# Kernel tuning notes

Measured on AMD Instinct MI355X. Metric: run time of the kernel, lower is better.

Reference implementation:

```python
import jax, jax.numpy as jnp
import numpy as np

NUM_EMBEDDINGS = 1024
EMBEDDING_DIM = 128
COMMITMENT_COEF = 0.25
DECAY = 0.99
EPS = 1e-5


def setup_inputs() -> dict:
    key = jax.random.key(0)
    k1, k2 = jax.random.split(key)
    z_e = jax.random.normal(k1, (64, EMBEDDING_DIM, 32, 32), dtype=jnp.float32)
    lim = 1.0 / NUM_EMBEDDINGS
    embed = jax.random.uniform(k2, (NUM_EMBEDDINGS, EMBEDDING_DIM), dtype=jnp.float32,
                               minval=-lim, maxval=lim)
    ema_cluster_size = jnp.zeros((NUM_EMBEDDINGS,), dtype=jnp.float32)
    ema_w = embed.copy()  # buffer initialized as clone of embed weights
    return {"z_e": z_e, "embed": embed,
            "ema_cluster_size": ema_cluster_size, "ema_w": ema_w}


def reference(z_e, embed, ema_cluster_size, ema_w):
    B, D, H, W = z_e.shape
    K = embed.shape[0]
    # [B,D,H,W] -> [N,D]
    flat = jnp.transpose(z_e, (0, 2, 3, 1)).reshape(-1, D)
    distances = (jnp.sum(flat ** 2, axis=1, keepdims=True)
                 + jnp.sum(embed ** 2, axis=1)
                 - 2.0 * jnp.matmul(flat, embed.T))
    encoding_indices = jnp.argmin(distances, axis=1)  # [N]

    quantized = embed[encoding_indices].reshape(B, H, W, D)
    quantized = jnp.transpose(quantized, (0, 3, 1, 2))  # [B,D,H,W]

    # ---- EMA codebook update (training path) ----
    N = flat.shape[0]
    cluster_size = jax.ops.segment_sum(jnp.ones((N,), flat.dtype),
                                       encoding_indices, num_segments=K)
    new_ema_cluster_size = DECAY * ema_cluster_size + (1.0 - DECAY) * cluster_size
    dw = jax.ops.segment_sum(flat, encoding_indices, num_segments=K)  # encodings^T @ flat
    new_ema_w = DECAY * ema_w + (1.0 - DECAY) * dw
    n = jnp.sum(new_ema_cluster_size)
    cs = (new_ema_cluster_size + EPS) / (n + K * EPS) * n
    new_embed = new_ema_w / cs[:, None]

    commitment_loss = jnp.mean((jax.lax.stop_gradient(quantized) - z_e) ** 2)
    loss = commitment_loss * COMMITMENT_COEF
    # straight-through estimator
    quantized_st = z_e + jax.lax.stop_gradient(quantized - z_e)
    indices = encoding_indices.reshape(B, H * W)
    return (quantized_st, indices, loss, new_embed, new_ema_cluster_size, new_ema_w)
```

## Files before the change

### kernel.cpp

```cpp
#include <hip/hip_runtime.h>

#define K_CODES 1024
#define DIM 128
#define HW 1024
#define NTOT 65536
#define DECAY 0.99f
#define OMD 0.01f
#define EPS 1e-5f
#define CCOEF 0.25f
#define MARGIN 1e-4f
#define FLCAP 24576

#define OFF_Q    0
#define OFF_IDX  8388608
#define OFF_LOSS (8388608 + 65536)
#define OFF_EMB  (OFF_LOSS + 1)
#define OFF_ECS  (OFF_EMB + 131072)
#define OFF_EMAW (OFF_ECS + 1024)

#define W_NORM2 0
#define W_RCP   1024
#define W_HIST  2048
#define W_LOSS  3072
#define W_FLCNT 3073
#define W_CNT2  3076
#define W_FL    (3076 + 24576)
#define W_M1F   (27652 + 24576)
#define W_CAND  (52228 + 24576)
#define W_EH    (76804 + 196608)
#define W_EL    (273412 + 65536)
#define W_NXIDX (338948 + 65536)
#define W_FLAT  (404484 + 65536)
#define W_NEED  (470020 + 8388608)

typedef __attribute__((ext_vector_type(8))) short short8v;
typedef __attribute__((ext_vector_type(4))) float f32x4;

__device__ __forceinline__ unsigned short f2bf(float f) {
    unsigned u = __float_as_uint(f);
    u += 0x7fffu + ((u >> 16) & 1u);
    return (unsigned short)(u >> 16);
}
__device__ __forceinline__ float bf2f(unsigned short h) {
    return __uint_as_float(((unsigned)h) << 16);
}

__global__ __launch_bounds__(256) void kzero(float* __restrict__ p, int n) {
    int i = blockIdx.x * 256 + threadIdx.x;
    if (i < n) p[i] = 0.f;
}

__device__ __forceinline__ float np_pairwise_sumsq_128(const float* p, size_t stride) {
    float r[8][4];
    #pragma unroll
    for (int j = 0; j < 8; ++j)
        #pragma unroll
        for (int L = 0; L < 4; ++L) {
            float x = p[(size_t)(j * 4 + L) * stride];
            r[j][L] = __fmul_rn(x, x);
        }
    #pragma unroll
    for (int c = 1; c < 4; ++c)
        #pragma unroll
        for (int j = 0; j < 8; ++j)
            #pragma unroll
            for (int L = 0; L < 4; ++L) {
                float x = p[(size_t)(c * 32 + j * 4 + L) * stride];
                r[j][L] = __fadd_rn(r[j][L], __fmul_rn(x, x));
            }
    float V[4];
    #pragma unroll
    for (int L = 0; L < 4; ++L) {
        float a = __fadd_rn(r[0][L], r[1][L]);
        float b = __fadd_rn(r[2][L], r[3][L]);
        float c2 = __fadd_rn(r[4][L], r[5][L]);
        float d2 = __fadd_rn(r[6][L], r[7][L]);
        V[L] = __fadd_rn(__fadd_rn(a, b), __fadd_rn(c2, d2));
    }
    return __fadd_rn(__fadd_rn(V[0], V[1]), __fadd_rn(V[2], V[3]));
}

__global__ __launch_bounds__(256) void kprep(
    const float* __restrict__ embed, float* __restrict__ norm2,
    unsigned short* __restrict__ ehs_g, unsigned short* __restrict__ els_g,
    float* __restrict__ zero_p, int zero_n)
{
    const int tid = threadIdx.x;
    const int bid = blockIdx.x;
    int zi = bid * 256 + tid;
    if (zi < zero_n) zero_p[zi] = 0.f;
    {
        const int g32 = tid >> 5, l32 = tid & 31;
        const int k = bid * 8 + g32;
        const float* row = embed + (size_t)k * DIM;
        float x = row[l32];
        float r = __fmul_rn(x, x);
        #pragma unroll
        for (int c = 1; c < 4; ++c) {
            float y = row[c * 32 + l32];
            r = __fadd_rn(r, __fmul_rn(y, y));
        }
        float s1 = __fadd_rn(r, __shfl_xor(r, 4, 64));
        float s2 = __fadd_rn(s1, __shfl_xor(s1, 8, 64));
        float s3 = __fadd_rn(s2, __shfl_xor(s2, 16, 64));
        float h1 = __fadd_rn(s3, __shfl_xor(s3, 1, 64));
        float h2 = __fadd_rn(h1, __shfl_xor(h1, 2, 64));
        if (l32 == 0) norm2[k] = h2;
    }
    if (ehs_g) {
        int hu = bid * 256 + tid;
        int U = hu >> 1, half = hu & 1;
        int code = U >> 4;
        int g = (U & 15) ^ (code & 15);
        const float* src = embed + (size_t)code * DIM + g * 8 + half * 4;
        float4 f = *(const float4*)src;
        unsigned short a = f2bf(f.x), b = f2bf(f.y), c = f2bf(f.z), d = f2bf(f.w);
        ushort4 hi; hi.x = a; hi.y = b; hi.z = c; hi.w = d;
        ushort4 lo;
        lo.x = f2bf(f.x - bf2f(a)); lo.y = f2bf(f.y - bf2f(b));
        lo.z = f2bf(f.z - bf2f(c)); lo.w = f2bf(f.w - bf2f(d));
        *(ushort4*)(ehs_g + (size_t)U * 8 + half * 4) = hi;
        *(ushort4*)(els_g + (size_t)U * 8 + half * 4) = lo;
    }
}

__global__ __launch_bounds__(256) void knx(const float* __restrict__ ze,
                                           float* __restrict__ nx,
                                           float* __restrict__ flat_c) {
    __shared__ float t[128][133];
    const int tid = threadIdx.x;
    const int n0 = blockIdx.x * 128;
    const int b = n0 >> 10, hw0 = n0 & (HW - 1);
    const float* zb = ze + (size_t)b * (DIM * HW) + hw0;
    #pragma unroll
    for (int i = 0; i < 64; ++i) {
        int d = i * 2 + (tid >> 7);
        int hw = tid & 127;
        t[hw][d] = zb[(size_t)d * HW + hw];
    }
    __syncthreads();
    if (tid < 128) nx[n0 + tid] = np_pairwise_sumsq_128(&t[tid][0], 1);
    if (flat_c) {
        #pragma unroll
        for (int i = 0; i < 16; ++i) {
            int lin = i * 256 + tid;
            int r  = lin >> 5;
            int c4 = lin & 31;
            float4 v = *(const float4*)&t[r][c4 * 4];
            *(float4*)&flat_c[(size_t)(n0 + r) * DIM + c4 * 4] = v;
        }
    }
}

__global__ __launch_bounds__(256, 4) void kapprox(
    const float* __restrict__ flat_c, const unsigned short* __restrict__ eh_g,
    const unsigned short* __restrict__ el_g, const float* __restrict__ norm2,
    int* __restrict__ idx_ws, float* __restrict__ idx_out,
    unsigned* __restrict__ hist, unsigned* __restrict__ flcnt,
    unsigned* __restrict__ fl_list, float* __restrict__ m1f)
{
    __shared__ __align__(16) unsigned short ehs[2][32 * 128];
    __shared__ __align__(16) unsigned short els[2][32 * 128];
    __shared__ float nes[1024];

    const int tid = threadIdx.x;
    const int l = tid & 63;
    const int w = tid >> 6;
    const int lg = l >> 4;
    const int lm = l & 15;
    const int n0 = blockIdx.x * 64;

    for (int i = tid; i < 1024; i += 256) nes[i] = norm2[i];

    short8v xh[4], xl[4];
    {
        const float* xr = flat_c + (size_t)(n0 + w * 16 + lm) * DIM;
        #pragma unroll
        for (int ks = 0; ks < 4; ++ks) {
            int kb = ks * 32 + lg * 8;
            float f0[8];
            *(float4*)&f0[0] = *(const float4*)(xr + kb);
            *(float4*)&f0[4] = *(const float4*)(xr + kb + 4);
            #pragma unroll
            for (int e = 0; e < 8; ++e) {
                unsigned short h0 = f2bf(f0[e]);
                xh[ks][e] = (short)h0;
                xl[ks][e] = (short)f2bf(f0[e] - bf2f(h0));
            }
        }
    }

    int roff[4];
    #pragma unroll
    for (int ks = 0; ks < 4; ++ks)
        roff[ks] = lm * 128 + (((ks * 4 + lg) ^ lm) * 8);

    const int su0 = tid * 8;
    const int su1 = 2048 + tid * 8;

    uint4 peh0 = *(const uint4*)(eh_g + su0);
    uint4 peh1 = *(const uint4*)(eh_g + su1);
    uint4 pel0 = *(const uint4*)(el_g + su0);
    uint4 pel1 = *(const uint4*)(el_g + su1);
    *(uint4*)&ehs[0][su0] = peh0;
    *(uint4*)&ehs[0][su1] = peh1;
    *(uint4*)&els[0][su0] = pel0;
    *(uint4*)&els[0][su1] = pel1;
    __syncthreads();

    float m1 = 3.4e38f, m2 = 3.4e38f;
    int c1 = 0;

    for (int it = 0; it < 32; ++it) {
        const int buf = it & 1;
        const int nt = it + 1;
        if (nt < 32) {
            const size_t nb = (size_t)nt * 4096;
            peh0 = *(const uint4*)(eh_g + nb + su0);
            peh1 = *(const uint4*)(eh_g + nb + su1);
            pel0 = *(const uint4*)(el_g + nb + su0);
            pel1 = *(const uint4*)(el_g + nb + su1);
        }
        f32x4 a00 = {0.f,0.f,0.f,0.f}, a01 = {0.f,0.f,0.f,0.f};
        const unsigned short* be = &ehs[buf][0];
        const unsigned short* bl = &els[buf][0];
        #pragma unroll
        for (int ks = 0; ks < 4; ++ks) {
            short8v eA = *(const short8v*)(be + roff[ks]);
            short8v lA = *(const short8v*)(bl + roff[ks]);
            short8v eB = *(const short8v*)(be + 2048 + roff[ks]);
            short8v lB = *(const short8v*)(bl + 2048 + roff[ks]);
            a00 = __builtin_amdgcn_mfma_f32_16x16x32_bf16(eA, xh[ks], a00, 0, 0, 0);
            a00 = __builtin_amdgcn_mfma_f32_16x16x32_bf16(lA, xh[ks], a00, 0, 0, 0);
            a00 = __builtin_amdgcn_mfma_f32_16x16x32_bf16(eA, xl[ks], a00, 0, 0, 0);
            a01 = __builtin_amdgcn_mfma_f32_16x16x32_bf16(eB, xh[ks], a01, 0, 0, 0);
            a01 = __builtin_amdgcn_mfma_f32_16x16x32_bf16(lB, xh[ks], a01, 0, 0, 0);
            a01 = __builtin_amdgcn_mfma_f32_16x16x32_bf16(eB, xl[ks], a01, 0, 0, 0);
        }
        #pragma unroll
        for (int r = 0; r < 4; ++r) {
            int code0 = it * 32 + lg * 4 + r;
            int code1 = code0 + 16;
            float s0 = nes[code0] - 2.f * a00[r];
            float s1 = nes[code1] - 2.f * a01[r];
            m2 = fminf(m2, fmaxf(m1, s0));
            if (s0 < m1) { m1 = s0; c1 = code0; }
            m2 = fminf(m2, fmaxf(m1, s1));
            if (s1 < m1) { m1 = s1; c1 = code1; }
        }
        if (nt < 32) {
            *(uint4*)&ehs[buf ^ 1][su0] = peh0;
            *(uint4*)&ehs[buf ^ 1][su1] = peh1;
            *(uint4*)&els[buf ^ 1][su0] = pel0;
            *(uint4*)&els[buf ^ 1][su1] = pel1;
        }
        __syncthreads();
    }

    #pragma unroll
    for (int mk = 16; mk <= 32; mk <<= 1) {
        float om1 = __shfl_xor(m1, mk, 64);
        int   oc1 = __shfl_xor(c1, mk, 64);
        float om2 = __shfl_xor(m2, mk, 64);
        m2 = fminf(fminf(m2, om2), fmaxf(m1, om1));
        if (om1 < m1 || (om1 == m1 && oc1 < c1)) { m1 = om1; c1 = oc1; }
    }
    if (lg == 0) {
        int n = n0 + w * 16 + lm;
        if (m2 - m1 > MARGIN) {
            idx_ws[n] = c1;
            idx_out[n] = (float)c1;
            atomicAdd(&hist[c1], 1u);
        } else {
            unsigned p = atomicAdd(flcnt, 1u);
            if (p < FLCAP) { fl_list[p] = (unsigned)n; m1f[p] = m1; }
            else {
                idx_ws[n] = c1; idx_out[n] = (float)c1;
                atomicAdd(&hist[c1], 1u);
            }
        }
    }
}

__global__ __launch_bounds__(256, 2) void kapprox2(
    const float* __restrict__ flat_c, const unsigned short* __restrict__ eh_g,
    const unsigned short* __restrict__ el_g, const float* __restrict__ norm2,
    const float* __restrict__ m1f, const unsigned* __restrict__ flcnt,
    const unsigned* __restrict__ fl_list, unsigned* __restrict__ cnt_g,
    unsigned* __restrict__ cand_g)
{
    __shared__ __align__(16) unsigned short ehs[2][32 * 128];
    __shared__ __align__(16) unsigned short els[2][32 * 128];
    __shared__ float nes[1024];
    __shared__ unsigned ccnt[128];
    __shared__ unsigned ccode[128][8];
    __shared__ int rid[128];
    __shared__ float thrs[128];

    const int tid = threadIdx.x;
    const int l = tid & 63;
    const int w = tid >> 6;
    const int lg = l >> 4;
    const int lm = l & 15;

    for (int i = tid; i < 1024; i += 256) nes[i] = norm2[i];

    int roff[4];
    #pragma unroll
    for (int ks = 0; ks < 4; ++ks)
        roff[ks] = lm * 128 + (((ks * 4 + lg) ^ lm) * 8);

    const int su0 = tid * 8;
    const int su1 = 2048 + tid * 8;

    unsigned nflag = flcnt[0];
    if (nflag > FLCAP) nflag = FLCAP;
    const unsigned nbat = (nflag + 127u) >> 7;
    const unsigned nwork = nbat * 8u;

    for (unsigned wi = blockIdx.x; wi < nwork; wi += gridDim.x) {
        const unsigned bat = wi >> 3;
        const int cq = (int)(wi & 7u);
        __syncthreads();
        if (tid < 128) {
            unsigned p = bat * 128u + tid;
            int n = (p < nflag) ? (int)fl_list[p] : -1;
            rid[tid] = n;
            thrs[tid] = (n >= 0) ? m1f[p] + MARGIN : -3.4e38f;
            ccnt[tid] = 0;
        }
        __syncthreads();

        const int lr0 = w * 32 + lm, lr1 = lr0 + 16;
        const int nr0 = rid[lr0], nr1 = rid[lr1];
        const float thr0 = thrs[lr0], thr1 = thrs[lr1];
        short8v xh0[4], xl0[4], xh1[4], xl1[4];
        {
            const float* xr0 = flat_c + (size_t)(nr0 < 0 ? 0 : nr0) * DIM;
            const float* xr1 = flat_c + (size_t)(nr1 < 0 ? 0 : nr1) * DIM;
            #pragma unroll
            for (int ks = 0; ks < 4; ++ks) {
                int kb = ks * 32 + lg * 8;
                float f0[8], f1[8];
                *(float4*)&f0[0] = *(const float4*)(xr0 + kb);
                *(float4*)&f0[4] = *(const float4*)(xr0 + kb + 4);
                *(float4*)&f1[0] = *(const float4*)(xr1 + kb);
                *(float4*)&f1[4] = *(const float4*)(xr1 + kb + 4);
                #pragma unroll
                for (int e = 0; e < 8; ++e) {
                    unsigned short h0 = f2bf(f0[e]);
                    unsigned short h1 = f2bf(f1[e]);
                    xh0[ks][e] = (short)h0;
                    xl0[ks][e] = (short)f2bf(f0[e] - bf2f(h0));
                    xh1[ks][e] = (short)h1;
                    xl1[ks][e] = (short)f2bf(f1[e] - bf2f(h1));
                }
            }
        }

        const int it0 = cq * 4;
        uint4 peh0, peh1, pel0, pel1;
        {
            const size_t nb = (size_t)it0 * 4096;
            peh0 = *(const uint4*)(eh_g + nb + su0);
            peh1 = *(const uint4*)(eh_g + nb + su1);
            pel0 = *(const uint4*)(el_g + nb + su0);
            pel1 = *(const uint4*)(el_g + nb + su1);
            *(uint4*)&ehs[0][su0] = peh0;
            *(uint4*)&ehs[0][su1] = peh1;
            *(uint4*)&els[0][su0] = pel0;
            *(uint4*)&els[0][su1] = pel1;
        }
        __syncthreads();

        for (int ii = 0; ii < 4; ++ii) {
            const int it = it0 + ii;
            const int buf = ii & 1;
            if (ii + 1 < 4) {
                const size_t nb = (size_t)(it + 1) * 4096;
                peh0 = *(const uint4*)(eh_g + nb + su0);
                peh1 = *(const uint4*)(eh_g + nb + su1);
                pel0 = *(const uint4*)(el_g + nb + su0);
                pel1 = *(const uint4*)(el_g + nb + su1);
            }
            f32x4 a00 = {0.f,0.f,0.f,0.f}, a01 = {0.f,0.f,0.f,0.f};
            f32x4 a10 = {0.f,0.f,0.f,0.f}, a11 = {0.f,0.f,0.f,0.f};
            const unsigned short* be = &ehs[buf][0];
            const unsigned short* bl = &els[buf][0];
            #pragma unroll
            for (int ks = 0; ks < 4; ++ks) {
                short8v eA = *(const short8v*)(be + roff[ks]);
                short8v lA = *(const short8v*)(bl + roff[ks]);
                short8v eB = *(const short8v*)(be + 2048 + roff[ks]);
                short8v lB = *(const short8v*)(bl + 2048 + roff[ks]);
                a00 = __builtin_amdgcn_mfma_f32_16x16x32_bf16(eA, xh0[ks], a00, 0, 0, 0);
                a00 = __builtin_amdgcn_mfma_f32_16x16x32_bf16(lA, xh0[ks], a00, 0, 0, 0);
                a00 = __builtin_amdgcn_mfma_f32_16x16x32_bf16(eA, xl0[ks], a00, 0, 0, 0);
                a10 = __builtin_amdgcn_mfma_f32_16x16x32_bf16(eA, xh1[ks], a10, 0, 0, 0);
                a10 = __builtin_amdgcn_mfma_f32_16x16x32_bf16(lA, xh1[ks], a10, 0, 0, 0);
                a10 = __builtin_amdgcn_mfma_f32_16x16x32_bf16(eA, xl1[ks], a10, 0, 0, 0);
                a01 = __builtin_amdgcn_mfma_f32_16x16x32_bf16(eB, xh0[ks], a01, 0, 0, 0);
                a01 = __builtin_amdgcn_mfma_f32_16x16x32_bf16(lB, xh0[ks], a01, 0, 0, 0);
                a01 = __builtin_amdgcn_mfma_f32_16x16x32_bf16(eB, xl0[ks], a01, 0, 0, 0);
                a11 = __builtin_amdgcn_mfma_f32_16x16x32_bf16(eB, xh1[ks], a11, 0, 0, 0);
                a11 = __builtin_amdgcn_mfma_f32_16x16x32_bf16(lB, xh1[ks], a11, 0, 0, 0);
                a11 = __builtin_amdgcn_mfma_f32_16x16x32_bf16(eB, xl1[ks], a11, 0, 0, 0);
            }
            #pragma unroll
            for (int r = 0; r < 4; ++r) {
                int code0 = it * 32 + lg * 4 + r;
                int code1 = code0 + 16;
                float s00 = nes[code0] - 2.f * a00[r];
                float s01 = nes[code1] - 2.f * a01[r];
                float s10 = nes[code0] - 2.f * a10[r];
                float s11 = nes[code1] - 2.f * a11[r];
                if (s00 <= thr0) {
                    unsigned p = atomicAdd(&ccnt[lr0], 1u);
                    if (p < 8) ccode[lr0][p] = (unsigned)code0;
                }
                if (s01 <= thr0) {
                    unsigned p = atomicAdd(&ccnt[lr0], 1u);
                    if (p < 8) ccode[lr0][p] = (unsigned)code1;
                }
                if (s10 <= thr1) {
                    unsigned p = atomicAdd(&ccnt[lr1], 1u);
                    if (p < 8) ccode[lr1][p] = (unsigned)code0;
                }
                if (s11 <= thr1) {
                    unsigned p = atomicAdd(&ccnt[lr1], 1u);
                    if (p < 8) ccode[lr1][p] = (unsigned)code1;
                }
            }
            if (ii + 1 < 4) {
                *(uint4*)&ehs[buf ^ 1][su0] = peh0;
                *(uint4*)&ehs[buf ^ 1][su1] = peh1;
                *(uint4*)&els[buf ^ 1][su0] = pel0;
                *(uint4*)&els[buf ^ 1][su1] = pel1;
            }
            __syncthreads();
        }

        if (tid < 128) {
            int n = rid[tid];
            unsigned lc = ccnt[tid];
            if (lc > 8u) lc = 8u;
            if (n >= 0 && lc > 0) {
                unsigned p = bat * 128u + tid;
                unsigned base = atomicAdd(&cnt_g[p], lc);
                for (unsigned j = 0; j < lc; ++j) {
                    unsigned slot = base + j;
                    if (slot < 8u) cand_g[(size_t)p * 8 + slot] = ccode[tid][j];
                }
            }
        }
    }
}

__global__ __launch_bounds__(256) void krescore(
    const float* __restrict__ flat_c, const float* __restrict__ embed,
    const float* __restrict__ norm2, const float* nxg,
    const unsigned* __restrict__ flcnt, const unsigned* __restrict__ fl_list,
    const unsigned* __restrict__ cnt_g, const unsigned* __restrict__ cand_g,
    int* idx_ws, float* __restrict__ idx_out, unsigned* __restrict__ hist)
{
    unsigned nflag = flcnt[0];
    if (nflag > FLCAP) nflag = FLCAP;
    for (unsigned p = blockIdx.x * 256u + threadIdx.x; p < nflag;
         p += gridDim.x * 256u) {
        const int n = (int)fl_list[p];
        unsigned c = cnt_g[p];
        if (c > 8u) c = 8u;
        unsigned cc[8];
        uint4 pk0 = *(const uint4*)(cand_g + (size_t)p * 8);
        uint4 pk1 = *(const uint4*)(cand_g + (size_t)p * 8 + 4);
        cc[0] = pk0.x; cc[1] = pk0.y; cc[2] = pk0.z; cc[3] = pk0.w;
        cc[4] = pk1.x; cc[5] = pk1.y; cc[6] = pk1.z; cc[7] = pk1.w;
        int bestk = (int)cc[0];
        if (c > 1) {
            float bests = 3.4e38f;
            bestk = 1 << 30;
            const float* xr = flat_c + (size_t)n * DIM;
            const float nx = nxg[n];
            #pragma unroll
            for (int q = 0; q < 8; ++q) {
                if (q < (int)c) {
                    int k = (int)cc[q];
                    const float* er = embed + (size_t)k * DIM;
                    float dot = 0.f;
                    #pragma unroll
                    for (int d4 = 0; d4 < 32; ++d4) {
                        float4 e4 = *(const float4*)(er + d4 * 4);
                        float4 x4 = *(const float4*)(xr + d4 * 4);
                        dot = fmaf(x4.x, e4.x, dot);
                        dot = fmaf(x4.y, e4.y, dot);
                        dot = fmaf(x4.z, e4.z, dot);
                        dot = fmaf(x4.w, e4.w, dot);
                    }
                    float qv = __fadd_rn(nx, norm2[k]);
                    float s = __fsub_rn(qv, __fmul_rn(2.f, dot));
                    if (s < bests || (s == bests && k < bestk)) { bests = s; bestk = k; }
                }
            }
        }
        idx_ws[n] = bestk;
        idx_out[n] = (float)bestk;
        atomicAdd(&hist[bestk], 1u);
    }
}

__global__ __launch_bounds__(256, 2) void kargmin(
    const float* __restrict__ ze, const float* __restrict__ embed,
    const float* __restrict__ norm2, const float* nxg,
    int* idx_ws, float* __restrict__ idx_out,
    unsigned int* __restrict__ hist)
{
    __shared__ float xs[128 * 36];
    __shared__ float es[128 * 36];
    __shared__ float nxs[128];
    const int tid = threadIdx.x;
    const int tx = tid & 15, ty = tid >> 4;
    const int n0 = blockIdx.x * 128;
    const float* zbase = ze + (size_t)(n0 >> 10) * (DIM * HW) + (n0 & (HW - 1));
    if (tid < 128) nxs[tid] = nxg[n0 + tid];
    float minv[8];
    int   mini[8];
    #pragma unroll
    for (int i = 0; i < 8; ++i) { minv[i] = 3.4e38f; mini[i] = 0; }
    for (int kt = 0; kt < 8; ++kt) {
        float acc[8][8];
        #pragma unroll
        for (int i = 0; i < 8; ++i)
            #pragma unroll
            for (int j = 0; j < 8; ++j) acc[i][j] = 0.f;
        for (int dc = 0; dc < 4; ++dc) {
            __syncthreads();
            #pragma unroll
            for (int it = 0; it < 4; ++it) {
                int lin = it * 256 + tid;
                int r  = lin & 127;
                int gu = lin >> 7;
                const float* gp = zbase + (size_t)(dc * 32 + gu * 4) * HW + r;
                float4 v;
                v.x = gp[0]; v.y = gp[HW]; v.z = gp[2 * HW]; v.w = gp[3 * HW];
                *(float4*)&xs[r * 36 + gu * 4] = v;
            }
            #pragma unroll
            for (int it = 0; it < 4; ++it) {
                int lin = it * 256 + tid;
                int k  = lin >> 3;
                int gu = lin & 7;
                float4 v = *(const float4*)(embed + (size_t)(kt * 128 + k) * DIM + dc * 32 + gu * 4);
                *(float4*)&es[k * 36 + gu * 4] = v;
            }
            __syncthreads();
            #pragma unroll
            for (int g = 0; g < 8; ++g) {
                float4 xf[8];
                #pragma unroll
                for (int i = 0; i < 8; ++i)
                    xf[i] = *(const float4*)&xs[(ty + i * 16) * 36 + g * 4];
                #pragma unroll
                for (int j = 0; j < 8; ++j) {
                    float4 ef = *(const float4*)&es[(tx + j * 16) * 36 + g * 4];
                    #pragma unroll
                    for (int i = 0; i < 8; ++i) {
                        acc[i][j] = fmaf(xf[i].x, ef.x, acc[i][j]);
                        acc[i][j] = fmaf(xf[i].y, ef.y, acc[i][j]);
                        acc[i][j] = fmaf(xf[i].z, ef.z, acc[i][j]);
                        acc[i][j] = fmaf(xf[i].w, ef.w, acc[i][j]);
                    }
                }
            }
        }
        #pragma unroll
        for (int j = 0; j < 8; ++j) {
            int kg = kt * 128 + tx + j * 16;
            float nrm = norm2[kg];
            #pragma unroll
            for (int i = 0; i < 8; ++i) {
                float q = __fadd_rn(nxs[ty + i * 16], nrm);
                float t = __fmul_rn(2.f, acc[i][j]);
                float s = __fsub_rn(q, t);
                if (s < minv[i]) { minv[i] = s; mini[i] = kg; }
            }
        }
    }
    #pragma unroll
    for (int i = 0; i < 8; ++i) {
        float v = minv[i]; int ix = mini[i];
        #pragma unroll
        for (int off = 8; off >= 1; off >>= 1) {
            float v2 = __shfl_xor(v, off, 16);
            int   i2 = __shfl_xor(ix, off, 16);
            if (v2 < v || (v2 == v && i2 < ix)) { v = v2; ix = i2; }
        }
        if (tx == 0) {
            int n = n0 + ty + i * 16;
            idx_ws[n] = ix;
            idx_out[n] = (float)ix;
            atomicAdd(&hist[ix], 1u);
        }
    }
}

__global__ __launch_bounds__(256) void kquant(
    const float* __restrict__ ze, const float* __restrict__ embed,
    const int* __restrict__ idx_ws, float* __restrict__ qout,
    float* __restrict__ dw_atomic, float* __restrict__ loss_acc)
{
    __shared__ float q[128 * 133];
    __shared__ int idxs[128];
    __shared__ float lsum[4];
    const int tid = threadIdx.x;
    const int n0 = blockIdx.x * 128;
    const int b = n0 >> 10;
    const int hw0 = n0 & (HW - 1);
    if (tid < 128) idxs[tid] = idx_ws[n0 + tid];
    __syncthreads();
    #pragma unroll
    for (int it = 0; it < 16; ++it) {
        int r = it * 8 + (tid >> 5);
        int c = tid & 31;
        float4 v = *(const float4*)(embed + (size_t)idxs[r] * DIM + c * 4);
        *(float4*)&q[r * 133 + c * 4] = v;
    }
    __syncthreads();
    const float* zb = ze + (size_t)b * (DIM * HW) + hw0;
    float* qb = qout + (size_t)b * (DIM * HW) + hw0;
    float lacc = 0.f;
    for (int dd = 0; dd < 64; ++dd) {
        int d = dd * 2 + (tid >> 7);
        int hw = tid & 127;
        float val = q[hw * 133 + d];
        size_t off = (size_t)d * HW + hw;
        float z = zb[off];
        qb[off] = val;
        float diff = val - z;
        lacc = fmaf(diff, diff, lacc);
        if (dw_atomic) atomicAdd(&dw_atomic[idxs[hw] * DIM + d], z);
    }
    #pragma unroll
    for (int off = 32; off >= 1; off >>= 1) lacc += __shfl_xor(lacc, off, 64);
    if ((tid & 63) == 0) lsum[tid >> 6] = lacc;
    __syncthreads();
    if (tid == 0) atomicAdd(loss_acc, lsum[0] + lsum[1] + lsum[2] + lsum[3]);
}

__global__ __launch_bounds__(512) void kdwf(
    const int* __restrict__ idx_ws, const float* __restrict__ flat_c,
    const float* __restrict__ ema_w, const float* __restrict__ rcp,
    float* __restrict__ out_emb, float* __restrict__ out_emaw)
{
    __shared__ float part[8][128];
    const int k = blockIdx.x;
    const int lane = threadIdx.x & 63;
    const int w = threadIdx.x >> 6;
    float lo = 0.f, hi = 0.f;
    const int nbeg = w * (NTOT / 8);
    const int nend = nbeg + (NTOT / 8);
    for (int base = nbeg; base < nend; base += 64) {
        int my = idx_ws[base + lane];
        unsigned long long m = __ballot(my == k);
        while (m) {
            int bit = __ffsll((long long)m) - 1;
            m &= m - 1;
            const float* row = flat_c + (size_t)(base + bit) * DIM;
            lo += row[lane];
            hi += row[lane + 64];
        }
    }
    part[w][lane] = lo;
    part[w][lane + 64] = hi;
    __syncthreads();
    if (w == 0) {
        float a = part[0][lane], b = part[0][lane + 64];
        #pragma unroll
        for (int u = 1; u < 8; ++u) {
            a += part[u][lane];
            b += part[u][lane + 64];
        }
        const float r = rcp[k];
        int elo = k * DIM + lane, ehi = elo + 64;
        float nwa = DECAY * ema_w[elo] + OMD * a;
        float nwb = DECAY * ema_w[ehi] + OMD * b;
        out_emaw[elo] = nwa;
        out_emaw[ehi] = nwb;
        out_emb[elo] = nwa * r;
        out_emb[ehi] = nwb * r;
    }
}

__global__ __launch_bounds__(256) void kfin1(
    const unsigned int* __restrict__ hist, const float* __restrict__ ema_cs,
    float* __restrict__ out_ecs, float* __restrict__ rcp,
    float* __restrict__ loss_out, const float* __restrict__ loss_acc)
{
    const int tid = threadIdx.x;
    __shared__ float wsum[4];
    float local = 0.f;
    float necs[4];
    #pragma unroll
    for (int u = 0; u < 4; ++u) {
        int k = u * 256 + tid;
        necs[u] = DECAY * ema_cs[k] + OMD * (float)hist[k];
        out_ecs[k] = necs[u];
        local += necs[u];
    }
    #pragma unroll
    for (int off = 32; off >= 1; off >>= 1) local += __shfl_xor(local, off, 64);
    if ((tid & 63) == 0) wsum[tid >> 6] = local;
    __syncthreads();
    float ntot = wsum[0] + wsum[1] + wsum[2] + wsum[3];
    #pragma unroll
    for (int u = 0; u < 4; ++u) {
        int k = u * 256 + tid;
        float cs = (necs[u] + EPS) / (ntot + (float)K_CODES * EPS) * ntot;
        rcp[k] = 1.f / cs;
    }
    if (tid == 0) loss_out[0] = loss_acc[0] * (CCOEF / (float)((size_t)NTOT * DIM));
}

__global__ __launch_bounds__(256) void kfin2(
    const float* __restrict__ ema_w, const float* __restrict__ dw,
    const float* __restrict__ rcp, float* __restrict__ out_emb,
    float* __restrict__ out_emaw)
{
    int e = blockIdx.x * 256 + threadIdx.x;
    int k = e >> 7;
    float nw = DECAY * ema_w[e] + OMD * dw[e];
    out_emaw[e] = nw;
    out_emb[e] = nw * rcp[k];
}

extern "C" void kernel_launch(void* const* d_in, const int* in_sizes, int n_in,
                              void* d_out, int out_size, void* d_ws, size_t ws_size,
                              hipStream_t stream) {
    const float* ze     = (const float*)d_in[0];
    const float* embed  = (const float*)d_in[1];
    const float* ema_cs = (const float*)d_in[2];
    const float* ema_w  = (const float*)d_in[3];
    float* out = (float*)d_out;

    float* ws = (float*)d_ws;
    float*          ws_norm2 = ws + W_NORM2;
    float*          ws_rcp   = ws + W_RCP;
    unsigned*       ws_hist  = (unsigned*)(ws + W_HIST);
    float*          ws_loss  = ws + W_LOSS;
    unsigned*       ws_flcnt = (unsigned*)(ws + W_FLCNT);
    unsigned*       ws_cnt   = (unsigned*)(ws + W_CNT2);
    unsigned*       ws_fl    = (unsigned*)(ws + W_FL);
    float*          ws_m1    = ws + W_M1F;
    unsigned*       ws_cand  = (unsigned*)(ws + W_CAND);
    float*          ws_dw    = ws + W_CAND;
    unsigned short* ws_eh    = (unsigned short*)(ws + W_EH);
    unsigned short* ws_el    = (unsigned short*)(ws + W_EL);
    float*          ws_nx    = ws + W_NXIDX;
    int*            ws_idx   = (int*)(ws + W_NXIDX);
    float*          ws_flat  = ws + W_FLAT;
    const size_t need = (size_t)W_NEED * sizeof(float);
    const bool big_ws = ws_size >= need;

    if (big_ws) {
        hipLaunchKernelGGL(kprep, dim3(128), dim3(256), 0, stream,
                           embed, ws_norm2, ws_eh, ws_el, (float*)ws_hist, 25604);
        hipLaunchKernelGGL(knx, dim3(512), dim3(256), 0, stream, ze, ws_nx, ws_flat);
        hipLaunchKernelGGL(kapprox, dim3(1024), dim3(256), 0, stream,
                           ws_flat, ws_eh, ws_el, ws_norm2,
                           ws_idx, out + OFF_IDX, ws_hist, ws_flcnt, ws_fl, ws_m1);
        hipLaunchKernelGGL(kapprox2, dim3(512), dim3(256), 0, stream,
                           ws_flat, ws_eh, ws_el, ws_norm2,
                           ws_m1, ws_flcnt, ws_fl, ws_cnt, ws_cand);
        hipLaunchKernelGGL(krescore, dim3(64), dim3(256), 0, stream,
                           ws_flat, embed, ws_norm2, ws_nx, ws_flcnt, ws_fl,
                           ws_cnt, ws_cand, ws_idx, out + OFF_IDX, ws_hist);
        hipLaunchKernelGGL(kquant, dim3(512), dim3(256), 0, stream,
                           ze, embed, ws_idx, out + OFF_Q, (float*)nullptr, ws_loss);
        hipLaunchKernelGGL(kfin1, dim3(1), dim3(256), 0, stream,
                           ws_hist, ema_cs, out + OFF_ECS, ws_rcp, out + OFF_LOSS, ws_loss);
        hipLaunchKernelGGL(kdwf, dim3(1024), dim3(512), 0, stream,
                           ws_idx, ws_flat, ema_w, ws_rcp,
                           out + OFF_EMB, out + OFF_EMAW);
    } else {
        hipLaunchKernelGGL(kprep, dim3(128), dim3(256), 0, stream,
                           embed, ws_norm2, (unsigned short*)nullptr,
                           (unsigned short*)nullptr, (float*)ws_hist, 1028);
        hipLaunchKernelGGL(kzero, dim3(512), dim3(256), 0, stream, ws_dw, 131072);
        hipLaunchKernelGGL(knx, dim3(512), dim3(256), 0, stream, ze, ws_nx, (float*)nullptr);
        hipLaunchKernelGGL(kargmin, dim3(512), dim3(256), 0, stream,
                           ze, embed, ws_norm2, ws_nx, ws_idx, out + OFF_IDX, ws_hist);
        hipLaunchKernelGGL(kquant, dim3(512), dim3(256), 0, stream,
                           ze, embed, ws_idx, out + OFF_Q, ws_dw, ws_loss);
        hipLaunchKernelGGL(kfin1, dim3(1), dim3(256), 0, stream,
                           ws_hist, ema_cs, out + OFF_ECS, ws_rcp, out + OFF_LOSS, ws_loss);
        hipLaunchKernelGGL(kfin2, dim3(512), dim3(256), 0, stream,
                           ema_w, ws_dw, ws_rcp, out + OFF_EMB, out + OFF_EMAW);
    }
}
```

Baseline: 183.0 us.

## Fuse prep kernels and merge quantize with dw-reduction into one tail grid

```diff
diff --git a/kernel.cpp b/kernel.cpp
--- a/kernel.cpp
+++ b/kernel.cpp
@@ -80,74 +80,73 @@
     return __fadd_rn(__fadd_rn(V[0], V[1]), __fadd_rn(V[2], V[3]));
 }
 
-__global__ __launch_bounds__(256) void kprep(
-    const float* __restrict__ embed, float* __restrict__ norm2,
-    unsigned short* __restrict__ ehs_g, unsigned short* __restrict__ els_g,
-    float* __restrict__ zero_p, int zero_n)
-{
+__global__ __launch_bounds__(256) void kpre(
+    const float* __restrict__ ze, float* __restrict__ nx,
+    float* __restrict__ flat_c, const float* __restrict__ embed,
+    float* __restrict__ norm2, unsigned short* __restrict__ ehs_g,
+    unsigned short* __restrict__ els_g, float* __restrict__ zero_p, int zero_n)
+{
+    __shared__ float t[128][133];
     const int tid = threadIdx.x;
     const int bid = blockIdx.x;
-    int zi = bid * 256 + tid;
-    if (zi < zero_n) zero_p[zi] = 0.f;
-    {
-        const int g32 = tid >> 5, l32 = tid & 31;
-        const int k = bid * 8 + g32;
-        const float* row = embed + (size_t)k * DIM;
-        float x = row[l32];
-        float r = __fmul_rn(x, x);
-        #pragma unroll
-        for (int c = 1; c < 4; ++c) {
-            float y = row[c * 32 + l32];
-            r = __fadd_rn(r, __fmul_rn(y, y));
-        }
-        float s1 = __fadd_rn(r, __shfl_xor(r, 4, 64));
-        float s2 = __fadd_rn(s1, __shfl_xor(s1, 8, 64));
-        float s3 = __fadd_rn(s2, __shfl_xor(s2, 16, 64));
-        float h1 = __fadd_rn(s3, __shfl_xor(s3, 1, 64));
-        float h2 = __fadd_rn(h1, __shfl_xor(h1, 2, 64));
-        if (l32 == 0) norm2[k] = h2;
-    }
-    if (ehs_g) {
-        int hu = bid * 256 + tid;
-        int U = hu >> 1, half = hu & 1;
-        int code = U >> 4;
-        int g = (U & 15) ^ (code & 15);
-        const float* src = embed + (size_t)code * DIM + g * 8 + half * 4;
-        float4 f = *(const float4*)src;
-        unsigned short a = f2bf(f.x), b = f2bf(f.y), c = f2bf(f.z), d = f2bf(f.w);
-        ushort4 hi; hi.x = a; hi.y = b; hi.z = c; hi.w = d;
-        ushort4 lo;
-        lo.x = f2bf(f.x - bf2f(a)); lo.y = f2bf(f.y - bf2f(b));
-        lo.z = f2bf(f.z - bf2f(c)); lo.w = f2bf(f.w - bf2f(d));
-        *(ushort4*)(ehs_g + (size_t)U * 8 + half * 4) = hi;
-        *(ushort4*)(els_g + (size_t)U * 8 + half * 4) = lo;
-    }
-}
-
-__global__ __launch_bounds__(256) void knx(const float* __restrict__ ze,
-                                           float* __restrict__ nx,
-                                           float* __restrict__ flat_c) {
-    __shared__ float t[128][133];
-    const int tid = threadIdx.x;
-    const int n0 = blockIdx.x * 128;
-    const int b = n0 >> 10, hw0 = n0 & (HW - 1);
-    const float* zb = ze + (size_t)b * (DIM * HW) + hw0;
-    #pragma unroll
-    for (int i = 0; i < 64; ++i) {
-        int d = i * 2 + (tid >> 7);
-        int hw = tid & 127;
-        t[hw][d] = zb[(size_t)d * HW + hw];
-    }
-    __syncthreads();
-    if (tid < 128) nx[n0 + tid] = np_pairwise_sumsq_128(&t[tid][0], 1);
-    if (flat_c) {
-        #pragma unroll
-        for (int i = 0; i < 16; ++i) {
-            int lin = i * 256 + tid;
-            int r  = lin >> 5;
-            int c4 = lin & 31;
-            float4 v = *(const float4*)&t[r][c4 * 4];
-            *(float4*)&flat_c[(size_t)(n0 + r) * DIM + c4 * 4] = v;
+    if (bid < 512) {
+        const int n0 = bid * 128;
+        const int b = n0 >> 10, hw0 = n0 & (HW - 1);
+        const float* zb = ze + (size_t)b * (DIM * HW) + hw0;
+        #pragma unroll
+        for (int i = 0; i < 64; ++i) {
+            int d = i * 2 + (tid >> 7);
+            int hw = tid & 127;
+            t[hw][d] = zb[(size_t)d * HW + hw];
+        }
+        __syncthreads();
+        if (tid < 128) nx[n0 + tid] = np_pairwise_sumsq_128(&t[tid][0], 1);
+        if (flat_c) {
+            #pragma unroll
+            for (int i = 0; i < 16; ++i) {
+                int lin = i * 256 + tid;
+                int r  = lin >> 5;
+                int c4 = lin & 31;
+                float4 v = *(const float4*)&t[r][c4 * 4];
+                *(float4*)&flat_c[(size_t)(n0 + r) * DIM + c4 * 4] = v;
+            }
+        }
+    } else {
+        const int pid = bid - 512;
+        int zi = pid * 256 + tid;
+        if (zi < zero_n) zero_p[zi] = 0.f;
+        {
+            const int g32 = tid >> 5, l32 = tid & 31;
+            const int k = pid * 8 + g32;
+            const float* row = embed + (size_t)k * DIM;
+            float x = row[l32];
+            float r = __fmul_rn(x, x);
+            #pragma unroll
+            for (int c = 1; c < 4; ++c) {
+                float y = row[c * 32 + l32];
+                r = __fadd_rn(r, __fmul_rn(y, y));
+            }
+            float s1 = __fadd_rn(r, __shfl_xor(r, 4, 64));
+            float s2 = __fadd_rn(s1, __shfl_xor(s1, 8, 64));
+            float s3 = __fadd_rn(s2, __shfl_xor(s2, 16, 64));
+            float h1 = __fadd_rn(s3, __shfl_xor(s3, 1, 64));
+            float h2 = __fadd_rn(h1, __shfl_xor(h1, 2, 64));
+            if (l32 == 0) norm2[k] = h2;
+        }
+        if (ehs_g) {
+            int hu = pid * 256 + tid;
+            int U = hu >> 1, half = hu & 1;
+            int code = U >> 4;
+            int g = (U & 15) ^ (code & 15);
+            const float* src = embed + (size_t)code * DIM + g * 8 + half * 4;
+            float4 f = *(const float4*)src;
+            unsigned short a = f2bf(f.x), b = f2bf(f.y), c = f2bf(f.z), d = f2bf(f.w);
+            ushort4 hi; hi.x = a; hi.y = b; hi.z = c; hi.w = d;
+            ushort4 lo;
+            lo.x = f2bf(f.x - bf2f(a)); lo.y = f2bf(f.y - bf2f(b));
+            lo.z = f2bf(f.z - bf2f(c)); lo.w = f2bf(f.w - bf2f(d));
+            *(ushort4*)(ehs_g + (size_t)U * 8 + half * 4) = hi;
+            *(ushort4*)(els_g + (size_t)U * 8 + half * 4) = lo;
         }
     }
 }
@@ -508,6 +507,131 @@
     }
 }
 
+__global__ __launch_bounds__(256) void kfin_r(
+    const unsigned int* __restrict__ hist, const float* __restrict__ ema_cs,
+    float* __restrict__ out_ecs, float* __restrict__ rcp)
+{
+    const int tid = threadIdx.x;
+    __shared__ float wsum[4];
+    float local = 0.f;
+    float necs[4];
+    #pragma unroll
+    for (int u = 0; u < 4; ++u) {
+        int k = u * 256 + tid;
+        necs[u] = DECAY * ema_cs[k] + OMD * (float)hist[k];
+        out_ecs[k] = necs[u];
+        local += necs[u];
+    }
+    #pragma unroll
+    for (int off = 32; off >= 1; off >>= 1) local += __shfl_xor(local, off, 64);
+    if ((tid & 63) == 0) wsum[tid >> 6] = local;
+    __syncthreads();
+    float ntot = wsum[0] + wsum[1] + wsum[2] + wsum[3];
+    #pragma unroll
+    for (int u = 0; u < 4; ++u) {
+        int k = u * 256 + tid;
+        float cs = (necs[u] + EPS) / (ntot + (float)K_CODES * EPS) * ntot;
+        rcp[k] = 1.f / cs;
+    }
+}
+
+__global__ __launch_bounds__(64) void kloss(
+    float* __restrict__ loss_out, const float* __restrict__ loss_acc)
+{
+    if (threadIdx.x == 0)
+        loss_out[0] = loss_acc[0] * (CCOEF / (float)((size_t)NTOT * DIM));
+}
+
+__global__ __launch_bounds__(512) void ktail(
+    const float* __restrict__ ze, const float* __restrict__ embed,
+    const int* __restrict__ idx_ws, float* __restrict__ qout,
+    float* __restrict__ loss_acc, const float* __restrict__ flat_c,
+    const float* __restrict__ ema_w, const float* __restrict__ rcp,
+    float* __restrict__ out_emb, float* __restrict__ out_emaw)
+{
+    __shared__ float shmem[64 * 133];
+    __shared__ int idxs[64];
+    __shared__ float lsum[8];
+    const int tid = threadIdx.x;
+    const int bid = blockIdx.x;
+    if (bid < 1024) {
+        const int n0 = bid * 64;
+        const int b = n0 >> 10;
+        const int hw0 = n0 & (HW - 1);
+        if (tid < 64) idxs[tid] = idx_ws[n0 + tid];
+        __syncthreads();
+        #pragma unroll
+        for (int it = 0; it < 4; ++it) {
+            int lin = it * 512 + tid;
+            int r = lin >> 5, c4 = lin & 31;
+            float4 v = *(const float4*)(embed + (size_t)idxs[r] * DIM + c4 * 4);
+            *(float4*)&shmem[r * 133 + c4 * 4] = v;
+        }
+        __syncthreads();
+        const float* zb = ze + (size_t)b * (DIM * HW) + hw0;
+        float* qb = qout + (size_t)b * (DIM * HW) + hw0;
+        const int hwl = tid & 63;
+        float lacc = 0.f;
+        #pragma unroll 4
+        for (int dd = 0; dd < 16; ++dd) {
+            int d = dd * 8 + (tid >> 6);
+            float val = shmem[hwl * 133 + d];
+            size_t off = (size_t)d * HW + hwl;
+            float z = zb[off];
+            qb[off] = val;
+            float diff = val - z;
+            lacc = fmaf(diff, diff, lacc);
+        }
+        #pragma unroll
+        for (int off = 32; off >= 1; off >>= 1) lacc += __shfl_xor(lacc, off, 64);
+        if ((tid & 63) == 0) lsum[tid >> 6] = lacc;
+        __syncthreads();
+        if (tid == 0) {
+            float s = ((lsum[0] + lsum[1]) + (lsum[2] + lsum[3]))
+                    + ((lsum[4] + lsum[5]) + (lsum[6] + lsum[7]));
+            atomicAdd(loss_acc, s);
+        }
+    } else {
+        float (*part)[128] = (float(*)[128])shmem;
+        const int k = bid - 1024;
+        const int lane = tid & 63;
+        const int w = tid >> 6;
+        float lo = 0.f, hi = 0.f;
+        const int nbeg = w * (NTOT / 8);
+        const int nend = nbeg + (NTOT / 8);
+        for (int base = nbeg; base < nend; base += 64) {
+            int my = idx_ws[base + lane];
+            unsigned long long m = __ballot(my == k);
+            while (m) {
+                int bit = __ffsll((long long)m) - 1;
+                m &= m - 1;
+                const float* row = flat_c + (size_t)(base + bit) * DIM;
+                lo += row[lane];
+                hi += row[lane + 64];
+            }
+        }
+        part[w][lane] = lo;
+        part[w][lane + 64] = hi;
+        __syncthreads();
+        if (w == 0) {
+            float a = part[0][lane], bsum = part[0][lane + 64];
+            #pragma unroll
+            for (int u = 1; u < 8; ++u) {
+                a += part[u][lane];
+                bsum += part[u][lane + 64];
+            }
+            const float r = rcp[k];
+            int elo = k * DIM + lane, ehi = elo + 64;
+            float nwa = DECAY * ema_w[elo] + OMD * a;
+            float nwb = DECAY * ema_w[ehi] + OMD * bsum;
+            out_emaw[elo] = nwa;
+            out_emaw[ehi] = nwb;
+            out_emb[elo] = nwa * r;
+            out_emb[ehi] = nwb * r;
+        }
+    }
+}
+
 __global__ __launch_bounds__(256, 2) void kargmin(
     const float* __restrict__ ze, const float* __restrict__ embed,
     const float* __restrict__ norm2, const float* nxg,
@@ -644,50 +768,6 @@
     if ((tid & 63) == 0) lsum[tid >> 6] = lacc;
     __syncthreads();
     if (tid == 0) atomicAdd(loss_acc, lsum[0] + lsum[1] + lsum[2] + lsum[3]);
-}
-
-__global__ __launch_bounds__(512) void kdwf(
-    const int* __restrict__ idx_ws, const float* __restrict__ flat_c,
-    const float* __restrict__ ema_w, const float* __restrict__ rcp,
-    float* __restrict__ out_emb, float* __restrict__ out_emaw)
-{
-    __shared__ float part[8][128];
-    const int k = blockIdx.x;
-    const int lane = threadIdx.x & 63;
-    const int w = threadIdx.x >> 6;
-    float lo = 0.f, hi = 0.f;
-    const int nbeg = w * (NTOT / 8);
-    const int nend = nbeg + (NTOT / 8);
-    for (int base = nbeg; base < nend; base += 64) {
-        int my = idx_ws[base + lane];
-        unsigned long long m = __ballot(my == k);
-        while (m) {
-            int bit = __ffsll((long long)m) - 1;
-            m &= m - 1;
-            const float* row = flat_c + (size_t)(base + bit) * DIM;
-            lo += row[lane];
-            hi += row[lane + 64];
-        }
-    }
-    part[w][lane] = lo;
-    part[w][lane + 64] = hi;
-    __syncthreads();
-    if (w == 0) {
-        float a = part[0][lane], b = part[0][lane + 64];
-        #pragma unroll
-        for (int u = 1; u < 8; ++u) {
-            a += part[u][lane];
-            b += part[u][lane + 64];
-        }
-        const float r = rcp[k];
-        int elo = k * DIM + lane, ehi = elo + 64;
-        float nwa = DECAY * ema_w[elo] + OMD * a;
-        float nwb = DECAY * ema_w[ehi] + OMD * b;
-        out_emaw[elo] = nwa;
-        out_emaw[ehi] = nwb;
-        out_emb[elo] = nwa * r;
-        out_emb[ehi] = nwb * r;
-    }
 }
 
 __global__ __launch_bounds__(256) void kfin1(
@@ -761,9 +841,9 @@
     const bool big_ws = ws_size >= need;
 
     if (big_ws) {
-        hipLaunchKernelGGL(kprep, dim3(128), dim3(256), 0, stream,
-                           embed, ws_norm2, ws_eh, ws_el, (float*)ws_hist, 25604);
-        hipLaunchKernelGGL(knx, dim3(512), dim3(256), 0, stream, ze, ws_nx, ws_flat);
+        hipLaunchKernelGGL(kpre, dim3(640), dim3(256), 0, stream,
+                           ze, ws_nx, ws_flat, embed, ws_norm2, ws_eh, ws_el,
+                           (float*)ws_hist, 25604);
         hipLaunchKernelGGL(kapprox, dim3(1024), dim3(256), 0, stream,
                            ws_flat, ws_eh, ws_el, ws_norm2,
                            ws_idx, out + OFF_IDX, ws_hist, ws_flcnt, ws_fl, ws_m1);
@@ -773,19 +853,19 @@
         hipLaunchKernelGGL(krescore, dim3(64), dim3(256), 0, stream,
                            ws_flat, embed, ws_norm2, ws_nx, ws_flcnt, ws_fl,
                            ws_cnt, ws_cand, ws_idx, out + OFF_IDX, ws_hist);
-        hipLaunchKernelGGL(kquant, dim3(512), dim3(256), 0, stream,
-                           ze, embed, ws_idx, out + OFF_Q, (float*)nullptr, ws_loss);
-        hipLaunchKernelGGL(kfin1, dim3(1), dim3(256), 0, stream,
-                           ws_hist, ema_cs, out + OFF_ECS, ws_rcp, out + OFF_LOSS, ws_loss);
-        hipLaunchKernelGGL(kdwf, dim3(1024), dim3(512), 0, stream,
-                           ws_idx, ws_flat, ema_w, ws_rcp,
-                           out + OFF_EMB, out + OFF_EMAW);
+        hipLaunchKernelGGL(kfin_r, dim3(1), dim3(256), 0, stream,
+                           ws_hist, ema_cs, out + OFF_ECS, ws_rcp);
+        hipLaunchKernelGGL(ktail, dim3(2048), dim3(512), 0, stream,
+                           ze, embed, ws_idx, out + OFF_Q, ws_loss,
+                           ws_flat, ema_w, ws_rcp, out + OFF_EMB, out + OFF_EMAW);
+        hipLaunchKernelGGL(kloss, dim3(1), dim3(64), 0, stream,
+                           out + OFF_LOSS, ws_loss);
     } else {
-        hipLaunchKernelGGL(kprep, dim3(128), dim3(256), 0, stream,
-                           embed, ws_norm2, (unsigned short*)nullptr,
-                           (unsigned short*)nullptr, (float*)ws_hist, 1028);
+        hipLaunchKernelGGL(kpre, dim3(640), dim3(256), 0, stream,
+                           ze, ws_nx, (float*)nullptr, embed, ws_norm2,
+                           (unsigned short*)nullptr, (unsigned short*)nullptr,
+                           (float*)ws_hist, 1028);
         hipLaunchKernelGGL(kzero, dim3(512), dim3(256), 0, stream, ws_dw, 131072);
-        hipLaunchKernelGGL(knx, dim3(512), dim3(256), 0, stream, ze, ws_nx, (float*)nullptr);
         hipLaunchKernelGGL(kargmin, dim3(512), dim3(256), 0, stream,
                            ze, embed, ws_norm2, ws_nx, ws_idx, out + OFF_IDX, ws_hist);
         hipLaunchKernelGGL(kquant, dim3(512), dim3(256), 0, stream,
```

Result: faster. 170.3 us, median of 3 (-6.9%).
